# Kernel tuning notes

Hardware: AMD Instinct MI355X
Metric: run time of the kernel (lower is better)

The kernel has to match this reference:

```python
import jax, jax.numpy as jnp
import numpy as np

N = 50000      # nodes
E = 800000     # edges (avg degree 16)
NF, EF, H, OUT, K = 16, 8, 64, 8, 3
N_MID = 2      # n_gnn_layers=4 -> first + 2 mid + last


def setup_inputs() -> dict:
    key = jax.random.key(0)
    ks = jax.random.split(key, 16)
    s = 0.05
    return {
        "x": jax.random.normal(ks[0], (N, NF), dtype=jnp.float32),
        "edge_index": jax.random.randint(ks[1], (2, E), 0, N, dtype=jnp.int64),
        "edge_attr": jax.random.normal(ks[2], (E, EF), dtype=jnp.float32),
        # edge_aggr MLP: Linear(EF,H) -> ReLU -> Linear(H,1)
        "mlp_W1": jax.random.normal(ks[3], (EF, H), dtype=jnp.float32) * s,
        "mlp_b1": jnp.zeros((H,), dtype=jnp.float32),
        "mlp_W2": jax.random.normal(ks[4], (H, 1), dtype=jnp.float32) * s,
        "mlp_b2": jnp.zeros((1,), dtype=jnp.float32),
        # TAGConv-style layers: K+1 linear maps each
        "W_first": jax.random.normal(ks[5], (K + 1, NF, H), dtype=jnp.float32) * s,
        "b_first": jnp.zeros((H,), dtype=jnp.float32),
        "W_mid": jax.random.normal(ks[6], (N_MID, K + 1, H, H), dtype=jnp.float32) * s,
        "b_mid": jnp.zeros((N_MID, H), dtype=jnp.float32),
        "W_last": jax.random.normal(ks[7], (K + 1, H, OUT), dtype=jnp.float32) * s,
        "b_last": jnp.zeros((OUT,), dtype=jnp.float32),
    }


def _gcn_norm(edge_weight, src, dst, n_nodes):
    # deg computed at target (col), D^{-1/2} A D^{-1/2}, no self loops
    deg = jax.ops.segment_sum(edge_weight, dst, num_segments=n_nodes)
    dinv = jnp.where(deg > 0, jax.lax.rsqrt(jnp.where(deg > 0, deg, 1.0)), 0.0)
    return dinv[src] * edge_weight * dinv[dst]  # [E]


def _tag_conv(x, Ws, b, src, dst, norm, n_nodes):
    # out = sum_k (A_norm^k x) W_k + b
    out = x @ Ws[0]
    h = x
    for k in range(1, Ws.shape[0]):
        h = jax.ops.segment_sum(h[src] * norm[:, None], dst, num_segments=n_nodes)
        out = out + h @ Ws[k]
    return out + b


def reference(x, edge_index, edge_attr, mlp_W1, mlp_b1, mlp_W2, mlp_b2,
              W_first, b_first, W_mid, b_mid, W_last, b_last):
    src, dst = edge_index[0], edge_index[1]
    n_nodes = x.shape[0]
    # edge MLP -> scalar edge weight per edge
    ew = (jax.nn.relu(edge_attr @ mlp_W1 + mlp_b1) @ mlp_W2 + mlp_b2)[:, 0]  # [E]
    norm = _gcn_norm(ew, src, dst, n_nodes)
    h = jax.nn.relu(_tag_conv(x, W_first, b_first, src, dst, norm, n_nodes))
    for i in range(W_mid.shape[0]):
        h = jax.nn.relu(_tag_conv(h, W_mid[i], b_mid[i], src, dst, norm, n_nodes))
    return _tag_conv(h, W_last, b_last, src, dst, norm, n_nodes)
```

## Files before the change

### kernel.cpp

```cpp
#include <hip/hip_runtime.h>
#include <stdint.h>

#define N_NODES 50000
#define N_EDGES 800000
#define NFEAT   16
#define EFEAT   8
#define HID     64
#define OUTF    8
#define NMID    2
#define NX      (N_NODES * NFEAT)
#define NPW     16
#define CAP     64
#define PGB     ((N_NODES + 4 * NPW - 1) / (4 * NPW))
#define PPB     ((N_NODES + 15) / 16)
#define NWB     ((N_NODES + 3) / 4)

typedef unsigned short ushort_t;
typedef unsigned int   uint_t;
typedef unsigned long long ull_t;
typedef __bf16 bf16x8 __attribute__((ext_vector_type(8)));
typedef float  f32x4  __attribute__((ext_vector_type(4)));

__device__ __forceinline__ float b2f(ushort_t u) {
    return __uint_as_float(((uint_t)u) << 16);
}
__device__ __forceinline__ ushort_t f2b(float f) {
    uint_t u = __float_as_uint(f);
    return (ushort_t)((u + 0x7fffu + ((u >> 16) & 1u)) >> 16);
}
__device__ __forceinline__ float h2f(ushort_t u) {
    union { ushort_t u; _Float16 h; } c; c.u = u; return (float)c.h;
}
__device__ __forceinline__ ushort_t f2h(float f) {
    union { ushort_t u; _Float16 h; } c; c.h = (_Float16)f; return c.u;
}

__global__ __launch_bounds__(256) void edge_mlp_kernel(
    const float* __restrict__ ea, const float* __restrict__ x,
    const int* __restrict__ ei,
    const float* __restrict__ W1, const float* __restrict__ b1,
    const float* __restrict__ W2, const float* __restrict__ b2,
    ushort_t* __restrict__ xb, float* __restrict__ ew,
    int* __restrict__ cnts, uint_t* __restrict__ bucket)
{
    __shared__ __align__(16) float W1t[EFEAT * HID];
    __shared__ __align__(8)  float2 b1w2[HID];
    __shared__ float b2s;
    int tid = threadIdx.x;
    for (int idx = tid; idx < EFEAT * HID; idx += 256) {
        int j = idx >> 3, i = idx & 7;
        W1t[idx] = W1[i * HID + j];
    }
    if (tid < HID) b1w2[tid] = make_float2(b1[tid], W2[tid]);
    if (tid == 0) b2s = b2[0];
    __syncthreads();

    int e = blockIdx.x * 256 + tid;
    if (e >= N_EDGES) return;

    xb[e] = f2b(x[e]);

    float4 v0 = ((const float4*)ea)[2 * e];
    float4 v1 = ((const float4*)ea)[2 * e + 1];

    float acc = b2s;
    #pragma unroll 2
    for (int j = 0; j < HID; ++j) {
        float4 wa = *(const float4*)&W1t[j * 8];
        float4 wb = *(const float4*)&W1t[j * 8 + 4];
        float2 bw = b1w2[j];
        float h = bw.x;
        h = fmaf(v0.x, wa.x, h); h = fmaf(v0.y, wa.y, h);
        h = fmaf(v0.z, wa.z, h); h = fmaf(v0.w, wa.w, h);
        h = fmaf(v1.x, wb.x, h); h = fmaf(v1.y, wb.y, h);
        h = fmaf(v1.z, wb.z, h); h = fmaf(v1.w, wb.w, h);
        acc = fmaf(fmaxf(h, 0.f), bw.y, acc);
    }
    ew[e] = acc;

    int d = ei[N_EDGES + e];
    int pos = atomicAdd(&cnts[d], 1);
    if (pos < CAP)
        bucket[(size_t)d * CAP + pos] = (uint_t)e;
}

__global__ __launch_bounds__(256) void degdinv_kernel(
    int* __restrict__ cnts, const uint_t* __restrict__ bucket,
    const float* __restrict__ ew, float* __restrict__ dinv)
{
    int tid = threadIdx.x;
    int n = blockIdx.x * 4 + (tid >> 6);
    int lane = tid & 63;
    if (n >= N_NODES) return;
    int c = cnts[n]; if (c > CAP) c = CAP;
    float w = 0.f;
    if (lane < c)
        w = ew[bucket[(size_t)n * CAP + lane]];
    #pragma unroll
    for (int o = 32; o; o >>= 1) w += __shfl_down(w, o, 64);
    if (lane == 0) {
        cnts[n] = c;
        dinv[n] = (w > 0.f) ? (1.f / sqrtf(w)) : 0.f;
    }
}

__global__ __launch_bounds__(256) void rescale_kernel(
    const int* __restrict__ cnts, const float* __restrict__ dinv,
    const float* __restrict__ ew, const int* __restrict__ ei,
    uint_t* __restrict__ bucket)
{
    int tid = threadIdx.x;
    int n = blockIdx.x * 4 + (tid >> 6);
    int lane = tid & 63;
    if (n >= N_NODES) return;
    int c = cnts[n];
    float dn = dinv[n];
    if (lane < c) {
        uint_t e = bucket[(size_t)n * CAP + lane];
        int s = ei[e];
        float nv = dinv[s] * ew[e] * dn;
        nv = fminf(fmaxf(nv, -60000.f), 60000.f);
        bucket[(size_t)n * CAP + lane] = (((uint_t)f2h(nv)) << 16) | (uint_t)s;
    }
}

template<int W>
__global__ __launch_bounds__(256, 6) void prop_kernel(
    const ushort_t* __restrict__ gsrc, ushort_t* __restrict__ gout,
    const int* __restrict__ cnts, const uint_t* __restrict__ bucket)
{
    int tid = threadIdx.x;
    int wv = tid >> 6, lane = tid & 63;
    int nb = (blockIdx.x * 4 + wv) * 4;
    if (nb >= N_NODES) return;

    int cv = (lane < 4) ? cnts[nb + lane] : 0;
    int c0 = __builtin_amdgcn_readlane(cv, 0);
    int c1 = __builtin_amdgcn_readlane(cv, 1);
    int c2 = __builtin_amdgcn_readlane(cv, 2);
    int c3 = __builtin_amdgcn_readlane(cv, 3);

    uint_t p0 = 0, p1 = 0, p2 = 0, p3 = 0;
    if (lane < c0) p0 = bucket[(size_t)(nb + 0) * CAP + lane];
    if (lane < c1) p1 = bucket[(size_t)(nb + 1) * CAP + lane];
    if (lane < c2) p2 = bucket[(size_t)(nb + 2) * CAP + lane];
    if (lane < c3) p3 = bucket[(size_t)(nb + 3) * CAP + lane];

    if (W == 64) {
        float s[4][4];
        #pragma unroll
        for (int n = 0; n < 4; ++n)
            #pragma unroll
            for (int k = 0; k < 4; ++k) s[n][k] = 0.f;

        int cq0 = c0 & ~3, cq1 = c1 & ~3, cq2 = c2 & ~3, cq3 = c3 & ~3;
        int cqm = max(max(cq0, cq1), max(cq2, cq3));

        for (int j = 0; j < cqm; j += 4) {
            #define GAT4(pN, cqN, n)                                                 \
                if (j < cqN) {                                                       \
                    _Pragma("unroll")                                                \
                    for (int k = 0; k < 4; ++k) {                                    \
                        int pe = __builtin_amdgcn_readlane((int)pN, j + k);          \
                        float nv = h2f((ushort_t)(((uint_t)pe) >> 16));              \
                        float h = b2f(gsrc[(size_t)(pe & 0xffff) * 64 + lane]);      \
                        s[n][k] = fmaf(h, nv, s[n][k]);                              \
                    }                                                                \
                }
            GAT4(p0, cq0, 0)
            GAT4(p1, cq1, 1)
            GAT4(p2, cq2, 2)
            GAT4(p3, cq3, 3)
            #undef GAT4
        }
        #define TAILG(pN, cqN, cN, n)                                                \
            for (int j = cqN; j < cN; ++j) {                                         \
                int pe = __builtin_amdgcn_readlane((int)pN, j);                      \
                float nv = h2f((ushort_t)(((uint_t)pe) >> 16));                      \
                float h = b2f(gsrc[(size_t)(pe & 0xffff) * 64 + lane]);              \
                s[n][0] = fmaf(h, nv, s[n][0]);                                      \
            }
        TAILG(p0, cq0, c0, 0)
        TAILG(p1, cq1, c1, 1)
        TAILG(p2, cq2, c2, 2)
        TAILG(p3, cq3, c3, 3)
        #undef TAILG

        #pragma unroll
        for (int n = 0; n < 4; ++n) {
            float v = (s[n][0] + s[n][1]) + (s[n][2] + s[n][3]);
            gout[(size_t)(nb + n) * 64 + lane] = f2b(v);
        }
    } else {
        const int il = lane & 15;
        const int quad = lane >> 4;
        #define PROC16(pN, cN, n)                                                    \
            {                                                                        \
                float s = 0.f;                                                       \
                for (int j = 0; j < cN; j += 4) {                                    \
                    int j4 = j + quad;                                               \
                    int pw = __shfl((int)pN, j4 & 63, 64);                           \
                    bool valid = j4 < cN;                                            \
                    int src = valid ? (pw & 0xffff) : 0;                             \
                    float nv = valid ? h2f((ushort_t)(((uint_t)pw) >> 16)) : 0.f;    \
                    float h = b2f(gsrc[(size_t)src * 16 + il]);                      \
                    s = fmaf(h, nv, s);                                              \
                }                                                                    \
                s += __shfl_xor(s, 16, 64);                                          \
                s += __shfl_xor(s, 32, 64);                                          \
                if (lane < 16) gout[(size_t)(nb + n) * 16 + lane] = f2b(s);          \
            }
        PROC16(p0, c0, 0)
        PROC16(p1, c1, 1)
        PROC16(p2, c2, 2)
        PROC16(p3, c3, 3)
        #undef PROC16
    }
}

template<int F32OUT>
__global__ __launch_bounds__(256, 8) void prop8_kernel(
    const ushort_t* __restrict__ gsrc, int GS, int GO,
    const ushort_t* __restrict__ add, int AS, int AO,
    ushort_t* __restrict__ outb, float* __restrict__ outf,
    const int* __restrict__ cnts, const uint_t* __restrict__ bucket)
{
    int tid = threadIdx.x;
    int wv = tid >> 6, lane = tid & 63;
    int nb = (blockIdx.x * 4 + wv) * 4;
    if (nb >= N_NODES) return;
    const int oct = lane >> 3, il = lane & 7;

    int cv = (lane < 4) ? cnts[nb + lane] : 0;
    int c0 = __builtin_amdgcn_readlane(cv, 0);
    int c1 = __builtin_amdgcn_readlane(cv, 1);
    int c2 = __builtin_amdgcn_readlane(cv, 2);
    int c3 = __builtin_amdgcn_readlane(cv, 3);

    uint_t p0 = 0, p1 = 0, p2 = 0, p3 = 0;
    if (lane < c0) p0 = bucket[(size_t)(nb + 0) * CAP + lane];
    if (lane < c1) p1 = bucket[(size_t)(nb + 1) * CAP + lane];
    if (lane < c2) p2 = bucket[(size_t)(nb + 2) * CAP + lane];
    if (lane < c3) p3 = bucket[(size_t)(nb + 3) * CAP + lane];

    #define PROC8(pN, cN, n)                                                         \
        {                                                                            \
            float s = 0.f;                                                           \
            for (int j = 0; j < cN; j += 8) {                                        \
                int jo = j + oct;                                                    \
                int pw = __shfl((int)pN, jo & 63, 64);                               \
                bool valid = jo < cN;                                                \
                int src = valid ? (pw & 0xffff) : 0;                                 \
                float nv = valid ? h2f((ushort_t)(((uint_t)pw) >> 16)) : 0.f;        \
                float h = b2f(gsrc[(size_t)src * GS + GO + il]);                     \
                s = fmaf(h, nv, s);                                                  \
            }                                                                        \
            s += __shfl_xor(s, 8, 64);                                               \
            s += __shfl_xor(s, 16, 64);                                              \
            s += __shfl_xor(s, 32, 64);                                              \
            if (lane < 8) {                                                          \
                float v = s + b2f(add[(size_t)(nb + n) * AS + AO + lane]);           \
                if (F32OUT) outf[(size_t)(nb + n) * 8 + lane] = v;                   \
                else        outb[(size_t)(nb + n) * 8 + lane] = f2b(v);              \
            }                                                                        \
        }
    PROC8(p0, c0, 0)
    PROC8(p1, c1, 1)
    PROC8(p2, c2, 2)
    PROC8(p3, c3, 3)
    #undef PROC8
}

template<int SRCW, int COUT, int ACT>
__global__ __launch_bounds__(256, 4) void gemm4_kernel(
    const ushort_t* __restrict__ s0, const ushort_t* __restrict__ s1,
    const ushort_t* __restrict__ s2, const ushort_t* __restrict__ s3,
    const float* __restrict__ Wg,
    const float* __restrict__ bias,
    ushort_t* __restrict__ outb)
{
    constexpr int NCH = (SRCW == 16) ? 2 : 8;
    constexpr int NT  = (COUT + 15) / 16;
    __shared__ __align__(16) ushort_t Bp[NCH * NT * 512];

    int tid = threadIdx.x;
    for (int idx = tid; idx < NCH * NT * 512; idx += 256) {
        int f = idx >> 9;
        int l = (idx >> 3) & 63, j = idx & 7;
        int ch = f / NT, nt = f - ch * NT;
        int kk = ((l >> 4) << 3) + j;
        int n = nt * 16 + (l & 15);
        int widx, krow;
        if (SRCW == 16) { widx = 2 * ch + (kk >> 4); krow = kk & 15; }
        else            { widx = ch >> 1;            krow = ((ch & 1) << 5) + kk; }
        float v = (n < COUT) ? Wg[((size_t)widx * SRCW + krow) * COUT + n] : 0.f;
        Bp[idx] = f2b(v);
    }
    __syncthreads();

    int wv = tid >> 6, lane = tid & 63;
    int node_base = (blockIdx.x * 4 + wv) * NPW;
    if (node_base >= N_NODES) return;
    int m = lane & 15, quad = lane >> 4;

    const ushort_t* srcs[4] = {s0, s1, s2, s3};
    bf16x8 a[NCH];
    #pragma unroll
    for (int ch = 0; ch < NCH; ++ch) {
        const ushort_t* sp;
        size_t off;
        if (SRCW == 16) {
            sp = (quad < 2) ? srcs[2 * ch] : srcs[2 * ch + 1];
            off = (size_t)(node_base + m) * 16 + (quad & 1) * 8;
        } else {
            sp = srcs[ch >> 1];
            off = (size_t)(node_base + m) * 64 + ((ch & 1) << 5) + quad * 8;
        }
        a[ch] = *(const bf16x8*)(sp + off);
    }

    #pragma unroll
    for (int nt = 0; nt < NT; ++nt) {
        float bv = bias[(nt * 16 + m) & (COUT - 1)];
        f32x4 c = {bv, bv, bv, bv};
        #pragma unroll
        for (int ch = 0; ch < NCH; ++ch) {
            bf16x8 b = *(const bf16x8*)&Bp[((ch * NT + nt) * 64 + lane) * 8];
            c = __builtin_amdgcn_mfma_f32_16x16x32_bf16(a[ch], b, c, 0, 0, 0);
        }
        #pragma unroll
        for (int r = 0; r < 4; ++r) {
            int row = node_base + quad * 4 + r;
            float v = ACT ? fmaxf(c[r], 0.f) : c[r];
            outb[(size_t)row * COUT + nt * 16 + m] = f2b(v);
        }
    }
}

__global__ __launch_bounds__(256, 4) void gemmL_kernel(
    const ushort_t* __restrict__ src,
    const float* __restrict__ Wl, const float* __restrict__ bl,
    ushort_t* __restrict__ Z)
{
    __shared__ __align__(16) ushort_t Bp[2 * 2 * 512];

    int tid = threadIdx.x;
    for (int idx = tid; idx < 2048; idx += 256) {
        int f = idx >> 9;
        int ch = f >> 1, nt = f & 1;
        int l = (idx >> 3) & 63, j = idx & 7;
        int kg = ch * 32 + ((l >> 4) << 3) + j;
        int n = nt * 16 + (l & 15);
        int widx = n >> 3, col = n & 7;
        Bp[idx] = f2b(Wl[((size_t)widx * 64 + kg) * 8 + col]);
    }
    __syncthreads();

    int wv = tid >> 6, lane = tid & 63;
    int node_base = (blockIdx.x * 4 + wv) * NPW;
    if (node_base >= N_NODES) return;
    int m = lane & 15, quad = lane >> 4;

    bf16x8 a[2];
    #pragma unroll
    for (int ch = 0; ch < 2; ++ch)
        a[ch] = *(const bf16x8*)(src + (size_t)(node_base + m) * 64 + ch * 32 + quad * 8);

    #pragma unroll
    for (int nt = 0; nt < 2; ++nt) {
        int n = nt * 16 + m;
        float bv = (n < 8) ? bl[n] : 0.f;
        f32x4 c = {bv, bv, bv, bv};
        #pragma unroll
        for (int ch = 0; ch < 2; ++ch) {
            bf16x8 b = *(const bf16x8*)&Bp[((ch * 2 + nt) * 64 + lane) * 8];
            c = __builtin_amdgcn_mfma_f32_16x16x32_bf16(a[ch], b, c, 0, 0, 0);
        }
        #pragma unroll
        for (int r = 0; r < 4; ++r) {
            int row = node_base + quad * 4 + r;
            Z[(size_t)row * 32 + n] = f2b(c[r]);
        }
    }
}

extern "C" void kernel_launch(void* const* d_in, const int* in_sizes, int n_in,
                              void* d_out, int out_size, void* d_ws, size_t ws_size,
                              hipStream_t stream)
{
    const float* x  = (const float*)d_in[0];
    const int*   ei = (const int*)d_in[1];
    const float* ea = (const float*)d_in[2];
    const float* W1 = (const float*)d_in[3];
    const float* b1 = (const float*)d_in[4];
    const float* W2 = (const float*)d_in[5];
    const float* b2 = (const float*)d_in[6];
    const float* Wf = (const float*)d_in[7];
    const float* bf = (const float*)d_in[8];
    const float* Wm = (const float*)d_in[9];
    const float* bm = (const float*)d_in[10];
    const float* Wl = (const float*)d_in[11];
    const float* bl = (const float*)d_in[12];

    char* ws = (char*)d_ws;
    size_t off = 0;
    auto take = [&](size_t bytes) -> char* {
        char* p = ws + off;
        off = (off + bytes + 255) & ~(size_t)255;
        return p;
    };
    int*      cnts   = (int*)take((size_t)N_NODES * 4);
    float*    dinv   = (float*)take((size_t)N_NODES * 4);
    float*    ew     = (float*)take((size_t)N_EDGES * 4);
    uint_t*   bucket = (uint_t*)take((size_t)N_NODES * CAP * 4);
    ushort_t* xb     = (ushort_t*)take((size_t)NX * 2 + 256);
    ushort_t* g1     = (ushort_t*)take((size_t)N_NODES * HID * 2 + 256);
    ushort_t* g2     = (ushort_t*)take((size_t)N_NODES * HID * 2 + 256);
    ushort_t* g3     = (ushort_t*)take((size_t)N_NODES * HID * 2 + 256);
    ushort_t* curA   = (ushort_t*)take((size_t)N_NODES * HID * 2 + 256);
    ushort_t* curB   = (ushort_t*)take((size_t)N_NODES * HID * 2 + 256);
    ushort_t* Z      = (ushort_t*)take((size_t)N_NODES * 32 * 2 + 256);
    ushort_t* t8a    = (ushort_t*)take((size_t)N_NODES * 8 * 2 + 256);
    ushort_t* t8b    = (ushort_t*)take((size_t)N_NODES * 8 * 2 + 256);

    hipMemsetAsync(cnts, 0, (size_t)N_NODES * 4, stream);

    const int EB = (N_EDGES + 255) / 256;

    edge_mlp_kernel<<<EB, 256, 0, stream>>>(ea, x, ei, W1, b1, W2, b2, xb, ew, cnts, bucket);
    degdinv_kernel<<<NWB, 256, 0, stream>>>(cnts, bucket, ew, dinv);
    rescale_kernel<<<NWB, 256, 0, stream>>>(cnts, dinv, ew, ei, bucket);

    prop_kernel<NFEAT><<<PPB, 256, 0, stream>>>(xb, g1, cnts, bucket);
    prop_kernel<NFEAT><<<PPB, 256, 0, stream>>>(g1, g2, cnts, bucket);
    prop_kernel<NFEAT><<<PPB, 256, 0, stream>>>(g2, g3, cnts, bucket);
    gemm4_kernel<NFEAT, HID, 1><<<PGB, 256, 0, stream>>>(
        xb, g1, g2, g3, Wf, bf, curA);

    ushort_t* cin = curA;
    ushort_t* cot = curB;
    for (int L = 0; L < NMID; ++L) {
        prop_kernel<HID><<<PPB, 256, 0, stream>>>(cin, g1, cnts, bucket);
        prop_kernel<HID><<<PPB, 256, 0, stream>>>(g1, g2, cnts, bucket);
        prop_kernel<HID><<<PPB, 256, 0, stream>>>(g2, g3, cnts, bucket);
        gemm4_kernel<HID, HID, 1><<<PGB, 256, 0, stream>>>(
            cin, g1, g2, g3, Wm + (size_t)L * 4 * HID * HID, bm + L * HID, cot);
        ushort_t* t = cin; cin = cot; cot = t;
    }

    gemmL_kernel<<<PGB, 256, 0, stream>>>(cin, Wl, bl, Z);
    prop8_kernel<0><<<PPB, 256, 0, stream>>>(Z, 32, 24, Z, 32, 16, t8a, nullptr, cnts, bucket);
    prop8_kernel<0><<<PPB, 256, 0, stream>>>(t8a, 8, 0, Z, 32, 8, t8b, nullptr, cnts, bucket);
    prop8_kernel<1><<<PPB, 256, 0, stream>>>(t8b, 8, 0, Z, 32, 0, nullptr, (float*)d_out, cnts, bucket);
}
```

Measured before the change: 458.8 us.

## Compact padded edge buckets into CSR with prefix-scanned row pointers

Adds a three-kernel prefix scan over the capped per-node counts to build a row pointer array. The rescale kernel now writes packed (norm, src) entries into a dense compact CSR array instead of back into the padded 64-slot buckets. All propagation kernels read neighbours through rowptr/compact. This replaces the padded layout, where each node's entries sat at a 256-byte stride, with contiguous storage, which should cut cache-line waste in the many prop passes. The cost is three extra small launches and a single-block scan step, which assumes NBLK is at most 256.

```diff
diff --git a/kernel.cpp b/kernel.cpp
--- a/kernel.cpp
+++ b/kernel.cpp
@@ -11,6 +11,7 @@
 #define NX      (N_NODES * NFEAT)
 #define NPW     16
 #define CAP     64
+#define NBLK    ((N_NODES + 255) / 256)
 #define PGB     ((N_NODES + 4 * NPW - 1) / (4 * NPW))
 #define PPB     ((N_NODES + 15) / 16)
 #define NWB     ((N_NODES + 3) / 4)
@@ -84,6 +85,58 @@
         bucket[(size_t)d * CAP + pos] = (uint_t)e;
 }
 
+__global__ __launch_bounds__(256) void bsum_kernel(const int* __restrict__ cnts,
+                                                   int* __restrict__ bsum) {
+    int t = threadIdx.x;
+    int i = blockIdx.x * 256 + t;
+    int v = (i < N_NODES) ? min(cnts[i], CAP) : 0;
+    #pragma unroll
+    for (int o = 32; o; o >>= 1) v += __shfl_down(v, o, 64);
+    __shared__ int ws4[4];
+    if ((t & 63) == 0) ws4[t >> 6] = v;
+    __syncthreads();
+    if (t == 0) bsum[blockIdx.x] = ws4[0] + ws4[1] + ws4[2] + ws4[3];
+}
+
+__global__ __launch_bounds__(256) void bscan_kernel(const int* __restrict__ bsum,
+                                                    int* __restrict__ boff,
+                                                    int* __restrict__ rowptr) {
+    __shared__ int sh[256];
+    int t = threadIdx.x;
+    int v = (t < NBLK) ? bsum[t] : 0;
+    sh[t] = v;
+    __syncthreads();
+    for (int o = 1; o < 256; o <<= 1) {
+        int val = sh[t];
+        int w = (t >= o) ? sh[t - o] : 0;
+        __syncthreads();
+        sh[t] = val + w;
+        __syncthreads();
+    }
+    if (t < NBLK) boff[t] = sh[t] - v;
+    if (t == NBLK - 1) rowptr[N_NODES] = sh[t];
+}
+
+__global__ __launch_bounds__(256) void rowptr_kernel(const int* __restrict__ cnts,
+                                                     const int* __restrict__ boff,
+                                                     int* __restrict__ rowptr) {
+    __shared__ int sh[256];
+    int t = threadIdx.x;
+    int i = blockIdx.x * 256 + t;
+    int v = (i < N_NODES) ? min(cnts[i], CAP) : 0;
+    sh[t] = v;
+    __syncthreads();
+    for (int o = 1; o < 256; o <<= 1) {
+        int val = sh[t];
+        int w = (t >= o) ? sh[t - o] : 0;
+        __syncthreads();
+        sh[t] = val + w;
+        __syncthreads();
+    }
+    int excl = sh[t] - v + boff[blockIdx.x];
+    if (i < N_NODES) rowptr[i] = excl;
+}
+
 __global__ __launch_bounds__(256) void degdinv_kernel(
     int* __restrict__ cnts, const uint_t* __restrict__ bucket,
     const float* __restrict__ ew, float* __restrict__ dinv)
@@ -107,7 +160,8 @@
 __global__ __launch_bounds__(256) void rescale_kernel(
     const int* __restrict__ cnts, const float* __restrict__ dinv,
     const float* __restrict__ ew, const int* __restrict__ ei,
-    uint_t* __restrict__ bucket)
+    const uint_t* __restrict__ bucket, const int* __restrict__ rowptr,
+    uint_t* __restrict__ compact)
 {
     int tid = threadIdx.x;
     int n = blockIdx.x * 4 + (tid >> 6);
@@ -115,36 +169,41 @@
     if (n >= N_NODES) return;
     int c = cnts[n];
     float dn = dinv[n];
+    int base = rowptr[n];
     if (lane < c) {
         uint_t e = bucket[(size_t)n * CAP + lane];
         int s = ei[e];
         float nv = dinv[s] * ew[e] * dn;
         nv = fminf(fmaxf(nv, -60000.f), 60000.f);
-        bucket[(size_t)n * CAP + lane] = (((uint_t)f2h(nv)) << 16) | (uint_t)s;
-    }
-}
+        compact[base + lane] = (((uint_t)f2h(nv)) << 16) | (uint_t)s;
+    }
+}
+
+#define CSR_PROLOG()                                                                 \
+    int rv = (lane < 5) ? rowptr[nb + lane] : 0;                                     \
+    int r0 = __builtin_amdgcn_readlane(rv, 0);                                       \
+    int r1 = __builtin_amdgcn_readlane(rv, 1);                                       \
+    int r2 = __builtin_amdgcn_readlane(rv, 2);                                       \
+    int r3 = __builtin_amdgcn_readlane(rv, 3);                                       \
+    int r4 = __builtin_amdgcn_readlane(rv, 4);                                       \
+    int c0 = r1 - r0, c1 = r2 - r1, c2 = r3 - r2, c3 = r4 - r3;                      \
+    uint_t p0 = 0, p1 = 0, p2 = 0, p3 = 0;                                           \
+    if (lane < c0) p0 = compact[r0 + lane];                                          \
+    if (lane < c1) p1 = compact[r1 + lane];                                          \
+    if (lane < c2) p2 = compact[r2 + lane];                                          \
+    if (lane < c3) p3 = compact[r3 + lane];
 
 template<int W>
 __global__ __launch_bounds__(256, 6) void prop_kernel(
     const ushort_t* __restrict__ gsrc, ushort_t* __restrict__ gout,
-    const int* __restrict__ cnts, const uint_t* __restrict__ bucket)
+    const int* __restrict__ rowptr, const uint_t* __restrict__ compact)
 {
     int tid = threadIdx.x;
     int wv = tid >> 6, lane = tid & 63;
     int nb = (blockIdx.x * 4 + wv) * 4;
     if (nb >= N_NODES) return;
 
-    int cv = (lane < 4) ? cnts[nb + lane] : 0;
-    int c0 = __builtin_amdgcn_readlane(cv, 0);
-    int c1 = __builtin_amdgcn_readlane(cv, 1);
-    int c2 = __builtin_amdgcn_readlane(cv, 2);
-    int c3 = __builtin_amdgcn_readlane(cv, 3);
-
-    uint_t p0 = 0, p1 = 0, p2 = 0, p3 = 0;
-    if (lane < c0) p0 = bucket[(size_t)(nb + 0) * CAP + lane];
-    if (lane < c1) p1 = bucket[(size_t)(nb + 1) * CAP + lane];
-    if (lane < c2) p2 = bucket[(size_t)(nb + 2) * CAP + lane];
-    if (lane < c3) p3 = bucket[(size_t)(nb + 3) * CAP + lane];
+    CSR_PROLOG()
 
     if (W == 64) {
         float s[4][4];
@@ -223,7 +282,7 @@
     const ushort_t* __restrict__ gsrc, int GS, int GO,
     const ushort_t* __restrict__ add, int AS, int AO,
     ushort_t* __restrict__ outb, float* __restrict__ outf,
-    const int* __restrict__ cnts, const uint_t* __restrict__ bucket)
+    const int* __restrict__ rowptr, const uint_t* __restrict__ compact)
 {
     int tid = threadIdx.x;
     int wv = tid >> 6, lane = tid & 63;
@@ -231,17 +290,7 @@
     if (nb >= N_NODES) return;
     const int oct = lane >> 3, il = lane & 7;
 
-    int cv = (lane < 4) ? cnts[nb + lane] : 0;
-    int c0 = __builtin_amdgcn_readlane(cv, 0);
-    int c1 = __builtin_amdgcn_readlane(cv, 1);
-    int c2 = __builtin_amdgcn_readlane(cv, 2);
-    int c3 = __builtin_amdgcn_readlane(cv, 3);
-
-    uint_t p0 = 0, p1 = 0, p2 = 0, p3 = 0;
-    if (lane < c0) p0 = bucket[(size_t)(nb + 0) * CAP + lane];
-    if (lane < c1) p1 = bucket[(size_t)(nb + 1) * CAP + lane];
-    if (lane < c2) p2 = bucket[(size_t)(nb + 2) * CAP + lane];
-    if (lane < c3) p3 = bucket[(size_t)(nb + 3) * CAP + lane];
+    CSR_PROLOG()
 
     #define PROC8(pN, cN, n)                                                         \
         {                                                                            \
@@ -409,47 +458,54 @@
         off = (off + bytes + 255) & ~(size_t)255;
         return p;
     };
-    int*      cnts   = (int*)take((size_t)N_NODES * 4);
-    float*    dinv   = (float*)take((size_t)N_NODES * 4);
-    float*    ew     = (float*)take((size_t)N_EDGES * 4);
-    uint_t*   bucket = (uint_t*)take((size_t)N_NODES * CAP * 4);
-    ushort_t* xb     = (ushort_t*)take((size_t)NX * 2 + 256);
-    ushort_t* g1     = (ushort_t*)take((size_t)N_NODES * HID * 2 + 256);
-    ushort_t* g2     = (ushort_t*)take((size_t)N_NODES * HID * 2 + 256);
-    ushort_t* g3     = (ushort_t*)take((size_t)N_NODES * HID * 2 + 256);
-    ushort_t* curA   = (ushort_t*)take((size_t)N_NODES * HID * 2 + 256);
-    ushort_t* curB   = (ushort_t*)take((size_t)N_NODES * HID * 2 + 256);
-    ushort_t* Z      = (ushort_t*)take((size_t)N_NODES * 32 * 2 + 256);
-    ushort_t* t8a    = (ushort_t*)take((size_t)N_NODES * 8 * 2 + 256);
-    ushort_t* t8b    = (ushort_t*)take((size_t)N_NODES * 8 * 2 + 256);
+    int*      cnts    = (int*)take((size_t)N_NODES * 4);
+    float*    dinv    = (float*)take((size_t)N_NODES * 4);
+    float*    ew      = (float*)take((size_t)N_EDGES * 4);
+    uint_t*   bucket  = (uint_t*)take((size_t)N_NODES * CAP * 4);
+    int*      rowptr  = (int*)take((size_t)(N_NODES + 1) * 4);
+    int*      bsum    = (int*)take((size_t)NBLK * 4);
+    int*      boff    = (int*)take((size_t)NBLK * 4);
+    uint_t*   compact = (uint_t*)take((size_t)N_EDGES * 4 + 256);
+    ushort_t* xb      = (ushort_t*)take((size_t)NX * 2 + 256);
+    ushort_t* g1      = (ushort_t*)take((size_t)N_NODES * HID * 2 + 256);
+    ushort_t* g2      = (ushort_t*)take((size_t)N_NODES * HID * 2 + 256);
+    ushort_t* g3      = (ushort_t*)take((size_t)N_NODES * HID * 2 + 256);
+    ushort_t* curA    = (ushort_t*)take((size_t)N_NODES * HID * 2 + 256);
+    ushort_t* curB    = (ushort_t*)take((size_t)N_NODES * HID * 2 + 256);
+    ushort_t* Z       = (ushort_t*)take((size_t)N_NODES * 32 * 2 + 256);
+    ushort_t* t8a     = (ushort_t*)take((size_t)N_NODES * 8 * 2 + 256);
+    ushort_t* t8b     = (ushort_t*)take((size_t)N_NODES * 8 * 2 + 256);
 
     hipMemsetAsync(cnts, 0, (size_t)N_NODES * 4, stream);
 
     const int EB = (N_EDGES + 255) / 256;
 
     edge_mlp_kernel<<<EB, 256, 0, stream>>>(ea, x, ei, W1, b1, W2, b2, xb, ew, cnts, bucket);
+    bsum_kernel<<<NBLK, 256, 0, stream>>>(cnts, bsum);
+    bscan_kernel<<<1, 256, 0, stream>>>(bsum, boff, rowptr);
+    rowptr_kernel<<<NBLK, 256, 0, stream>>>(cnts, boff, rowptr);
     degdinv_kernel<<<NWB, 256, 0, stream>>>(cnts, bucket, ew, dinv);
-    rescale_kernel<<<NWB, 256, 0, stream>>>(cnts, dinv, ew, ei, bucket);
-
-    prop_kernel<NFEAT><<<PPB, 256, 0, stream>>>(xb, g1, cnts, bucket);
-    prop_kernel<NFEAT><<<PPB, 256, 0, stream>>>(g1, g2, cnts, bucket);
-    prop_kernel<NFEAT><<<PPB, 256, 0, stream>>>(g2, g3, cnts, bucket);
+    rescale_kernel<<<NWB, 256, 0, stream>>>(cnts, dinv, ew, ei, bucket, rowptr, compact);
+
+    prop_kernel<NFEAT><<<PPB, 256, 0, stream>>>(xb, g1, rowptr, compact);
+    prop_kernel<NFEAT><<<PPB, 256, 0, stream>>>(g1, g2, rowptr, compact);
+    prop_kernel<NFEAT><<<PPB, 256, 0, stream>>>(g2, g3, rowptr, compact);
     gemm4_kernel<NFEAT, HID, 1><<<PGB, 256, 0, stream>>>(
         xb, g1, g2, g3, Wf, bf, curA);
 
     ushort_t* cin = curA;
     ushort_t* cot = curB;
     for (int L = 0; L < NMID; ++L) {
-        prop_kernel<HID><<<PPB, 256, 0, stream>>>(cin, g1, cnts, bucket);
-        prop_kernel<HID><<<PPB, 256, 0, stream>>>(g1, g2, cnts, bucket);
-        prop_kernel<HID><<<PPB, 256, 0, stream>>>(g2, g3, cnts, bucket);
+        prop_kernel<HID><<<PPB, 256, 0, stream>>>(cin, g1, rowptr, compact);
+        prop_kernel<HID><<<PPB, 256, 0, stream>>>(g1, g2, rowptr, compact);
+        prop_kernel<HID><<<PPB, 256, 0, stream>>>(g2, g3, rowptr, compact);
         gemm4_kernel<HID, HID, 1><<<PGB, 256, 0, stream>>>(
             cin, g1, g2, g3, Wm + (size_t)L * 4 * HID * HID, bm + L * HID, cot);
         ushort_t* t = cin; cin = cot; cot = t;
     }
 
     gemmL_kernel<<<PGB, 256, 0, stream>>>(cin, Wl, bl, Z);
-    prop8_kernel<0><<<PPB, 256, 0, stream>>>(Z, 32, 24, Z, 32, 16, t8a, nullptr, cnts, bucket);
-    prop8_kernel<0><<<PPB, 256, 0, stream>>>(t8a, 8, 0, Z, 32, 8, t8b, nullptr, cnts, bucket);
-    prop8_kernel<1><<<PPB, 256, 0, stream>>>(t8b, 8, 0, Z, 32, 0, nullptr, (float*)d_out, cnts, bucket);
-}
+    prop8_kernel<0><<<PPB, 256, 0, stream>>>(Z, 32, 24, Z, 32, 16, t8a, nullptr, rowptr, compact);
+    prop8_kernel<0><<<PPB, 256, 0, stream>>>(t8a, 8, 0, Z, 32, 8, t8b, nullptr, rowptr, compact);
+    prop8_kernel<1><<<PPB, 256, 0, stream>>>(t8b, 8, 0, Z, 32, 0, nullptr, (float*)d_out, rowptr, compact);
+}
```

Result: slower. 484.7 us (+5.7%).
